# Kernel optimization log

Hardware: AMD Instinct MI355X
Metric: run time of the kernel (lower is better)

The kernel has to match this reference:

```python
import jax, jax.numpy as jnp
import numpy as np


def segsum(x):
    # x: (..., T). Returns (..., T, T) with out[l, s] = sum_{i=s+1..l} x[i] for s <= l, -inf above diagonal.
    T = x.shape[-1]
    cs = jnp.cumsum(x, axis=-1)
    diff = cs[..., :, None] - cs[..., None, :]
    mask = jnp.tril(jnp.ones((T, T), dtype=bool))
    return jnp.where(mask, diff, -jnp.inf)


def ssd_forward(X, A, B, C, block_len):
    # X: (b, s, h, p); A: (b, s, h); B, C: (b, s, h, n)
    b, s, h, p = X.shape
    n = B.shape[-1]
    nc = s // block_len  # number of chunks
    Xb = X.reshape(b, nc, block_len, h, p)
    Bb = B.reshape(b, nc, block_len, h, n)
    Cb = C.reshape(b, nc, block_len, h, n)
    Ab = A.reshape(b, nc, block_len, h).transpose(0, 3, 1, 2)  # (b, h, c, l)

    A_cumsum = jnp.cumsum(Ab, axis=-1)  # (b, h, c, l)

    # 1. Intra-chunk (diagonal block) outputs
    L = jnp.exp(segsum(Ab))  # (b, h, c, l, s)
    Y_diag = jnp.einsum('bclhn,bcshn,bhcls,bcshp->bclhp', Cb, Bb, L, Xb)

    # 2. Per-chunk final states
    decay_states = jnp.exp(A_cumsum[..., -1:] - A_cumsum)  # (b, h, c, l)
    states = jnp.einsum('bclhn,bhcl,bclhp->bchpn', Bb, decay_states, Xb)

    # 3. Inter-chunk scan (initial state = 0)
    init = jnp.zeros_like(states[:, :1])
    states_cat = jnp.concatenate([init, states], axis=1)  # (b, c+1, h, p, n)
    A_last = A_cumsum[..., -1]  # (b, h, c)
    A_padded = jnp.pad(A_last, ((0, 0), (0, 0), (1, 0)))  # (b, h, c+1)
    decay_chunk = jnp.exp(segsum(A_padded))  # (b, h, c+1, c+1)
    new_states = jnp.einsum('bhzc,bchpn->bzhpn', decay_chunk, states_cat)
    states_in = new_states[:, :-1]  # state entering each chunk, (b, c, h, p, n)

    # 4. Off-diagonal (inter-chunk) contribution to outputs
    state_decay_out = jnp.exp(A_cumsum)  # (b, h, c, l)
    Y_off = jnp.einsum('bclhn,bchpn,bhcl->bclhp', Cb, states_in, state_decay_out)

    return (Y_diag + Y_off).reshape(b, s, h, p)


def setup_inputs() -> dict:
    key = jax.random.key(0)
    k1, k2, k3, k4 = jax.random.split(key, 4)
    b, s, h, p, n = 16, 1024, 32, 64, 128
    X = jax.random.normal(k1, (b, s, h, p), dtype=jnp.float32)
    A = -jax.random.uniform(k2, (b, s, h), dtype=jnp.float32)  # negative decay (discretized dt*A)
    B = jax.random.normal(k3, (b, s, h, n), dtype=jnp.float32)
    C = jax.random.normal(k4, (b, s, h, n), dtype=jnp.float32)
    return {'X': X, 'A': A, 'B': B, 'C': C, 'block_len': 64}


def reference(X, A, B, C, block_len):
    return ssd_forward(X, A, B, C, block_len)
```

## Files before the change

### kernel.cpp

```cpp
#include <hip/hip_runtime.h>

typedef __attribute__((ext_vector_type(8))) __bf16 bf16x8;
typedef __attribute__((ext_vector_type(4))) __bf16 bf16x4;
typedef __attribute__((ext_vector_type(4))) float f32x4;

#define SEQ 1024
#define NH 32
#define PD 64
#define ND 128
#define CLEN 64
#define NCHUNK 16

#define CS_LD 136
#define BT_LD 72
#define XT_LD 72
#define SS_LD 72
#define SR_LD 136

__device__ __forceinline__ int swz(int r) { return ((r >> 2) & 7) << 3; }

__device__ __forceinline__ void barrier_lds() {
    asm volatile("s_waitcnt lgkmcnt(0)" ::: "memory");
    __builtin_amdgcn_s_barrier();
    asm volatile("" ::: "memory");
}

__global__ __launch_bounds__(512, 2)
void ssd_fused(const float* __restrict__ Xg, const float* __restrict__ Ag,
               const float* __restrict__ Bg, const float* __restrict__ Cg,
               float* __restrict__ Yg)
{
    __shared__ __align__(16) float cumA[64];
    __shared__ __align__(16) float eA[64];
    __shared__ __align__(16) float dxA[64];
    __shared__ __align__(16) float scal[4];
    __shared__ __align__(16) __bf16 Cs[64 * CS_LD];
    __shared__ __align__(16) __bf16 BsT[128 * BT_LD];
    __shared__ __align__(16) __bf16 XsT[64 * XT_LD];
    __shared__ __align__(16) __bf16 Ss[64 * SS_LD];
    __shared__ __align__(16) __bf16 SrB[64 * SR_LD];

    const int tid  = threadIdx.x;
    const int w    = tid >> 6;
    const int lane = tid & 63;
    const int q    = lane >> 4;
    const int ln   = lane & 15;
    const int m4   = w & 3;
    const int h2   = w >> 2;

    const int bh = blockIdx.x;
    const int b  = bh >> 5;
    const int h  = bh & 31;

    const float* Xb = Xg + (size_t)b * SEQ * NH * PD + (size_t)h * PD;
    const float* Ab = Ag + (size_t)b * SEQ * NH + h;
    const float* Bb = Bg + (size_t)b * SEQ * NH * ND + (size_t)h * ND;
    const float* Cb = Cg + (size_t)b * SEQ * NH * ND + (size_t)h * ND;
    float*       Yb = Yg + (size_t)b * SEQ * NH * PD + (size_t)h * PD;

    {
        unsigned int* p0 = (unsigned int*)SrB;
        for (int i = tid; i < 64 * SR_LD / 2; i += 512) p0[i] = 0u;
    }
    f32x4 srun[4];
    #pragma unroll
    for (int t = 0; t < 4; ++t) srun[t] = (f32x4){0.f, 0.f, 0.f, 0.f};
    __syncthreads();

    f32x4 creg[4], breg[4], xreg[2];
    float areg = 0.f;
    #define LOAD_CHUNK(S0) do {                                                   \
        _Pragma("unroll")                                                         \
        for (int i = 0; i < 4; ++i) {                                             \
            int v   = tid + 512 * i;                                              \
            int row = v >> 5;                                                     \
            int c4  = (v & 31) << 2;                                              \
            creg[i] = *(const f32x4*)(Cb + (size_t)((S0) + row) * (NH * ND) + c4);\
            breg[i] = *(const f32x4*)(Bb + (size_t)((S0) + row) * (NH * ND) + c4);\
        }                                                                         \
        _Pragma("unroll")                                                         \
        for (int i = 0; i < 2; ++i) {                                             \
            int v   = tid + 512 * i;                                              \
            int row = v >> 4;                                                     \
            int c4  = (v & 15) << 2;                                              \
            xreg[i] = *(const f32x4*)(Xb + (size_t)((S0) + row) * (NH * PD) + c4);\
        }                                                                         \
        if (w == 0) areg = Ab[(size_t)((S0) + lane) * NH];                        \
    } while (0)

    LOAD_CHUNK(0);

    for (int c = 0; c < NCHUNK; ++c) {
        const int s0 = c * CLEN;

        #pragma unroll
        for (int i = 0; i < 4; ++i) {
            int v   = tid + 512 * i;
            int row = v >> 5;
            int c4  = (v & 31) << 2;
            bf16x4 cv;
            cv[0] = (__bf16)creg[i][0]; cv[1] = (__bf16)creg[i][1];
            cv[2] = (__bf16)creg[i][2]; cv[3] = (__bf16)creg[i][3];
            *(bf16x4*)&Cs[row * CS_LD + c4] = cv;
            #pragma unroll
            for (int j = 0; j < 4; ++j) {
                int n = c4 + j;
                BsT[n * BT_LD + (row ^ swz(n))] = (__bf16)breg[i][j];
            }
        }
        #pragma unroll
        for (int i = 0; i < 2; ++i) {
            int v   = tid + 512 * i;
            int row = v >> 4;
            int c4  = (v & 15) << 2;
            #pragma unroll
            for (int j = 0; j < 4; ++j) {
                int p = c4 + j;
                XsT[p * XT_LD + (row ^ swz(p))] = (__bf16)xreg[i][j];
            }
        }

        if (w == 0) {
            float v = areg;
            #pragma unroll
            for (int off = 1; off < 64; off <<= 1) {
                float u = __shfl_up(v, off, 64);
                if (lane >= off) v += u;
            }
            float alast = __shfl(v, 63, 64);
            cumA[lane] = v;
            eA[lane]   = __expf(v);
            dxA[lane]  = __expf(alast - v);
            if (lane == 0) scal[0] = __expf(alast);
        }

        if (c + 1 < NCHUNK) LOAD_CHUNK((c + 1) * CLEN);

        barrier_lds();

        {
            const int arow = 16 * m4 + ln;
            f32x4 ca = *(const f32x4*)&cumA[16 * m4 + 4 * q];
            #pragma unroll
            for (int t = 0; t < 2; ++t) {
                const int sn   = 2 * h2 + t;
                const int scol = 16 * sn + ln;
                if (sn <= m4) {
                    f32x4 acc = (f32x4){0.f, 0.f, 0.f, 0.f};
                    #pragma unroll
                    for (int kt = 0; kt < 4; ++kt) {
                        bf16x8 af = *(const bf16x8*)&Cs[arow * CS_LD + kt * 32 + q * 8];
                        bf16x8 bq;
                        #pragma unroll
                        for (int j = 0; j < 8; ++j) {
                            int n = kt * 32 + q * 8 + j;
                            bq[j] = BsT[n * BT_LD + (scol ^ swz(n))];
                        }
                        acc = __builtin_amdgcn_mfma_f32_16x16x32_bf16(af, bq, acc, 0, 0, 0);
                    }
                    float csc = cumA[scol];
                    #pragma unroll
                    for (int r = 0; r < 4; ++r) {
                        int lrow  = 16 * m4 + 4 * q + r;
                        float val = (lrow >= scol) ? acc[r] * __expf(ca[r] - csc) : 0.f;
                        Ss[lrow * SS_LD + scol] = (__bf16)val;
                    }
                } else {
                    #pragma unroll
                    for (int r = 0; r < 4; ++r)
                        Ss[(16 * m4 + 4 * q + r) * SS_LD + scol] = (__bf16)0.f;
                }
            }
        }

        barrier_lds();

        f32x4 yacc[2], yoff[2];
        yacc[0] = (f32x4){0.f, 0.f, 0.f, 0.f};
        yacc[1] = (f32x4){0.f, 0.f, 0.f, 0.f};
        yoff[0] = (f32x4){0.f, 0.f, 0.f, 0.f};
        yoff[1] = (f32x4){0.f, 0.f, 0.f, 0.f};
        {
            const int arow = 16 * m4 + ln;
            for (int kt = 0; kt <= (m4 >> 1); ++kt) {
                bf16x8 af = *(const bf16x8*)&Ss[arow * SS_LD + kt * 32 + q * 8];
                #pragma unroll
                for (int t = 0; t < 2; ++t) {
                    int prow = 16 * (2 * h2 + t) + ln;
                    bf16x8 bq = *(const bf16x8*)&XsT[prow * XT_LD + ((kt * 32 + q * 8) ^ swz(prow))];
                    yacc[t] = __builtin_amdgcn_mfma_f32_16x16x32_bf16(af, bq, yacc[t], 0, 0, 0);
                }
            }
            #pragma unroll
            for (int kt = 0; kt < 4; ++kt) {
                bf16x8 craw = *(const bf16x8*)&Cs[arow * CS_LD + kt * 32 + q * 8];
                #pragma unroll
                for (int t = 0; t < 2; ++t) {
                    int pt = 2 * h2 + t;
                    bf16x8 bq = *(const bf16x8*)&SrB[(16 * pt + ln) * SR_LD + kt * 32 + q * 8];
                    yoff[t] = __builtin_amdgcn_mfma_f32_16x16x32_bf16(craw, bq, yoff[t], 0, 0, 0);
                }
            }
            f32x4 ev = *(const f32x4*)&eA[16 * m4 + 4 * q];
            #pragma unroll
            for (int t = 0; t < 2; ++t)
                #pragma unroll
                for (int r = 0; r < 4; ++r)
                    yacc[t][r] += ev[r] * yoff[t][r];
        }

        f32x4 sacc[4];
        #pragma unroll
        for (int t = 0; t < 4; ++t) sacc[t] = (f32x4){0.f, 0.f, 0.f, 0.f};
        {
            const int prow = 16 * m4 + ln;
            #pragma unroll
            for (int kt = 0; kt < 2; ++kt) {
                bf16x8 xv = *(const bf16x8*)&XsT[prow * XT_LD + ((kt * 32 + q * 8) ^ swz(prow))];
                f32x4 d0 = *(const f32x4*)&dxA[kt * 32 + q * 8];
                f32x4 d1 = *(const f32x4*)&dxA[kt * 32 + q * 8 + 4];
                bf16x8 af;
                #pragma unroll
                for (int j = 0; j < 4; ++j) {
                    af[j]     = (__bf16)((float)xv[j] * d0[j]);
                    af[4 + j] = (__bf16)((float)xv[4 + j] * d1[j]);
                }
                #pragma unroll
                for (int t = 0; t < 4; ++t) {
                    int nrow = 16 * (4 * h2 + t) + ln;
                    bf16x8 bq = *(const bf16x8*)&BsT[nrow * BT_LD + ((kt * 32 + q * 8) ^ swz(nrow))];
                    sacc[t] = __builtin_amdgcn_mfma_f32_16x16x32_bf16(af, bq, sacc[t], 0, 0, 0);
                }
            }
        }

        barrier_lds();

        {
            float elast = scal[0];
            #pragma unroll
            for (int t = 0; t < 4; ++t) {
                int ncol = 16 * (4 * h2 + t) + ln;
                #pragma unroll
                for (int r = 0; r < 4; ++r) {
                    float s = elast * srun[t][r] + sacc[t][r];
                    srun[t][r] = s;
                    SrB[(16 * m4 + 4 * q + r) * SR_LD + ncol] = (__bf16)s;
                }
            }
            #pragma unroll
            for (int t = 0; t < 2; ++t) {
                int pcol = 16 * (2 * h2 + t) + ln;
                #pragma unroll
                for (int r = 0; r < 4; ++r) {
                    int lrow = 16 * m4 + 4 * q + r;
                    Yb[(size_t)(s0 + lrow) * (NH * PD) + pcol] = yacc[t][r];
                }
            }
        }

        barrier_lds();
    }
    #undef LOAD_CHUNK
}

extern "C" void kernel_launch(void* const* d_in, const int* in_sizes, int n_in,
                              void* d_out, int out_size, void* d_ws, size_t ws_size,
                              hipStream_t stream) {
    const float* X = (const float*)d_in[0];
    const float* A = (const float*)d_in[1];
    const float* B = (const float*)d_in[2];
    const float* C = (const float*)d_in[3];
    float* Y = (float*)d_out;
    dim3 grid(512, 1, 1), block(512, 1, 1);
    hipLaunchKernelGGL(ssd_fused, grid, block, 0, stream, X, A, B, C, Y);
}
```

Baseline: 644.0 us.

## Load C fragments directly to registers and restructure chunk pipeline stages

C is no longer staged through shared memory; each lane loads its MFMA A-fragment rows of C straight from global memory into registers and converts them to bf16 there. B is now stored in both row-major and transposed shared layouts, so the C·Bᵀ product uses vector LDS reads instead of eight scalar gathers. The loop is reordered so that staging and the cumsum scan for the next chunk happen at the end of the current iteration, and the C prefetch is issued later, which moves one barrier. The occupancy hint in launch bounds rises from 2 to 4, which caps registers per thread more tightly and risks spills.

```diff
diff --git a/kernel.cpp b/kernel.cpp
--- a/kernel.cpp
+++ b/kernel.cpp
@@ -11,7 +11,7 @@
 #define CLEN 64
 #define NCHUNK 16
 
-#define CS_LD 136
+#define BS_LD 136
 #define BT_LD 72
 #define XT_LD 72
 #define SS_LD 72
@@ -25,7 +25,7 @@
     asm volatile("" ::: "memory");
 }
 
-__global__ __launch_bounds__(512, 2)
+__global__ __launch_bounds__(512, 4)
 void ssd_fused(const float* __restrict__ Xg, const float* __restrict__ Ag,
                const float* __restrict__ Bg, const float* __restrict__ Cg,
                float* __restrict__ Yg)
@@ -34,10 +34,10 @@
     __shared__ __align__(16) float eA[64];
     __shared__ __align__(16) float dxA[64];
     __shared__ __align__(16) float scal[4];
-    __shared__ __align__(16) __bf16 Cs[64 * CS_LD];
+    __shared__ __align__(16) __bf16 Bs [64 * BS_LD];
     __shared__ __align__(16) __bf16 BsT[128 * BT_LD];
     __shared__ __align__(16) __bf16 XsT[64 * XT_LD];
-    __shared__ __align__(16) __bf16 Ss[64 * SS_LD];
+    __shared__ __align__(16) __bf16 Ss [64 * SS_LD];
     __shared__ __align__(16) __bf16 SrB[64 * SR_LD];
 
     const int tid  = threadIdx.x;
@@ -58,6 +58,8 @@
     const float* Cb = Cg + (size_t)b * SEQ * NH * ND + (size_t)h * ND;
     float*       Yb = Yg + (size_t)b * SEQ * NH * PD + (size_t)h * PD;
 
+    const int arow = 16 * m4 + ln;
+
     {
         unsigned int* p0 = (unsigned int*)SrB;
         for (int i = tid; i < 64 * SR_LD / 2; i += 512) p0[i] = 0u;
@@ -65,17 +67,18 @@
     f32x4 srun[4];
     #pragma unroll
     for (int t = 0; t < 4; ++t) srun[t] = (f32x4){0.f, 0.f, 0.f, 0.f};
-    __syncthreads();
-
-    f32x4 creg[4], breg[4], xreg[2];
+
+    f32x4 breg[4], xreg[2];
     float areg = 0.f;
-    #define LOAD_CHUNK(S0) do {                                                   \
+    f32x4 cf32[8];
+    bf16x8 cfrag[4];
+
+    #define LOADBX(S0) do {                                                       \
         _Pragma("unroll")                                                         \
         for (int i = 0; i < 4; ++i) {                                             \
             int v   = tid + 512 * i;                                              \
             int row = v >> 5;                                                     \
             int c4  = (v & 31) << 2;                                              \
-            creg[i] = *(const f32x4*)(Cb + (size_t)((S0) + row) * (NH * ND) + c4);\
             breg[i] = *(const f32x4*)(Bb + (size_t)((S0) + row) * (NH * ND) + c4);\
         }                                                                         \
         _Pragma("unroll")                                                         \
@@ -88,59 +91,88 @@
         if (w == 0) areg = Ab[(size_t)((S0) + lane) * NH];                        \
     } while (0)
 
-    LOAD_CHUNK(0);
+    #define LOADC(S0) do {                                                        \
+        _Pragma("unroll")                                                         \
+        for (int kt = 0; kt < 4; ++kt) {                                          \
+            const float* p = Cb + (size_t)((S0) + arow) * (NH * ND) + kt * 32 + q * 8; \
+            cf32[2 * kt]     = *(const f32x4*)(p);                                \
+            cf32[2 * kt + 1] = *(const f32x4*)(p + 4);                            \
+        }                                                                         \
+    } while (0)
+
+    #define STAGE() do {                                                          \
+        _Pragma("unroll")                                                         \
+        for (int i = 0; i < 4; ++i) {                                             \
+            int v   = tid + 512 * i;                                              \
+            int row = v >> 5;                                                     \
+            int c4  = (v & 31) << 2;                                              \
+            bf16x4 bv;                                                            \
+            bv[0] = (__bf16)breg[i][0]; bv[1] = (__bf16)breg[i][1];               \
+            bv[2] = (__bf16)breg[i][2]; bv[3] = (__bf16)breg[i][3];               \
+            *(bf16x4*)&Bs[row * BS_LD + c4] = bv;                                 \
+            _Pragma("unroll")                                                     \
+            for (int j = 0; j < 4; ++j) {                                         \
+                int n = c4 + j;                                                   \
+                BsT[n * BT_LD + (row ^ swz(n))] = bv[j];                          \
+            }                                                                     \
+        }                                                                         \
+        _Pragma("unroll")                                                         \
+        for (int i = 0; i < 2; ++i) {                                             \
+            int v   = tid + 512 * i;                                              \
+            int row = v >> 4;                                                     \
+            int c4  = (v & 15) << 2;                                              \
+            _Pragma("unroll")                                                     \
+            for (int j = 0; j < 4; ++j) {                                         \
+                int p = c4 + j;                                                   \
+                XsT[p * XT_LD + (row ^ swz(p))] = (__bf16)xreg[i][j];             \
+            }                                                                     \
+        }                                                                         \
+    } while (0)
+
+    #define SCAN() do {                                                           \
+        if (w == 0) {                                                             \
+            float v = areg;                                                       \
+            _Pragma("unroll")                                                     \
+            for (int off = 1; off < 64; off <<= 1) {                              \
+                float u = __shfl_up(v, off, 64);                                  \
+                if (lane >= off) v += u;                                          \
+            }                                                                     \
+            float alast = __shfl(v, 63, 64);                                      \
+            cumA[lane] = v;                                                       \
+            eA[lane]   = __expf(v);                          \
+            dxA[lane]  = __expf(alast - v);                   \
+            if (lane == 0) scal[0] = __expf(alast);                               \
+        }                                                                         \
+    } while (0)
+
+    LOADBX(0);
+    LOADC(0);
+    STAGE();
+    SCAN();
 
     for (int c = 0; c < NCHUNK; ++c) {
         const int s0 = c * CLEN;
 
+        barrier_lds();
+
+        const float elast = scal[0];
+        const f32x4 ev = *(const f32x4*)&eA[16 * m4 + 4 * q];
+        const f32x4 ca = *(const f32x4*)&cumA[16 * m4 + 4 * q];
+
+        if (c + 1 < NCHUNK) LOADBX((c + 1) * CLEN);
+
         #pragma unroll
-        for (int i = 0; i < 4; ++i) {
-            int v   = tid + 512 * i;
-            int row = v >> 5;
-            int c4  = (v & 31) << 2;
-            bf16x4 cv;
-            cv[0] = (__bf16)creg[i][0]; cv[1] = (__bf16)creg[i][1];
-            cv[2] = (__bf16)creg[i][2]; cv[3] = (__bf16)creg[i][3];
-            *(bf16x4*)&Cs[row * CS_LD + c4] = cv;
+        for (int kt = 0; kt < 4; ++kt) {
+            bf16x8 f;
             #pragma unroll
             for (int j = 0; j < 4; ++j) {
-                int n = c4 + j;
-                BsT[n * BT_LD + (row ^ swz(n))] = (__bf16)breg[i][j];
-            }
-        }
-        #pragma unroll
-        for (int i = 0; i < 2; ++i) {
-            int v   = tid + 512 * i;
-            int row = v >> 4;
-            int c4  = (v & 15) << 2;
-            #pragma unroll
-            for (int j = 0; j < 4; ++j) {
-                int p = c4 + j;
-                XsT[p * XT_LD + (row ^ swz(p))] = (__bf16)xreg[i][j];
-            }
-        }
-
-        if (w == 0) {
-            float v = areg;
-            #pragma unroll
-            for (int off = 1; off < 64; off <<= 1) {
-                float u = __shfl_up(v, off, 64);
-                if (lane >= off) v += u;
-            }
-            float alast = __shfl(v, 63, 64);
-            cumA[lane] = v;
-            eA[lane]   = __expf(v);
-            dxA[lane]  = __expf(alast - v);
-            if (lane == 0) scal[0] = __expf(alast);
-        }
-
-        if (c + 1 < NCHUNK) LOAD_CHUNK((c + 1) * CLEN);
-
-        barrier_lds();
+                f[j]     = (__bf16)cf32[2 * kt][j];
+                f[4 + j] = (__bf16)cf32[2 * kt + 1][j];
+            }
+            cfrag[kt] = f;
+        }
 
         {
-            const int arow = 16 * m4 + ln;
-            f32x4 ca = *(const f32x4*)&cumA[16 * m4 + 4 * q];
             #pragma unroll
             for (int t = 0; t < 2; ++t) {
                 const int sn   = 2 * h2 + t;
@@ -149,14 +181,8 @@
                     f32x4 acc = (f32x4){0.f, 0.f, 0.f, 0.f};
                     #pragma unroll
                     for (int kt = 0; kt < 4; ++kt) {
-                        bf16x8 af = *(const bf16x8*)&Cs[arow * CS_LD + kt * 32 + q * 8];
-                        bf16x8 bq;
-                        #pragma unroll
-                        for (int j = 0; j < 8; ++j) {
-                            int n = kt * 32 + q * 8 + j;
-                            bq[j] = BsT[n * BT_LD + (scol ^ swz(n))];
-                        }
-                        acc = __builtin_amdgcn_mfma_f32_16x16x32_bf16(af, bq, acc, 0, 0, 0);
+                        bf16x8 bq = *(const bf16x8*)&Bs[scol * BS_LD + kt * 32 + q * 8];
+                        acc = __builtin_amdgcn_mfma_f32_16x16x32_bf16(cfrag[kt], bq, acc, 0, 0, 0);
                     }
                     float csc = cumA[scol];
                     #pragma unroll
@@ -173,47 +199,24 @@
             }
         }
 
-        barrier_lds();
-
-        f32x4 yacc[2], yoff[2];
-        yacc[0] = (f32x4){0.f, 0.f, 0.f, 0.f};
-        yacc[1] = (f32x4){0.f, 0.f, 0.f, 0.f};
+        f32x4 yoff[2];
         yoff[0] = (f32x4){0.f, 0.f, 0.f, 0.f};
         yoff[1] = (f32x4){0.f, 0.f, 0.f, 0.f};
-        {
-            const int arow = 16 * m4 + ln;
-            for (int kt = 0; kt <= (m4 >> 1); ++kt) {
-                bf16x8 af = *(const bf16x8*)&Ss[arow * SS_LD + kt * 32 + q * 8];
-                #pragma unroll
-                for (int t = 0; t < 2; ++t) {
-                    int prow = 16 * (2 * h2 + t) + ln;
-                    bf16x8 bq = *(const bf16x8*)&XsT[prow * XT_LD + ((kt * 32 + q * 8) ^ swz(prow))];
-                    yacc[t] = __builtin_amdgcn_mfma_f32_16x16x32_bf16(af, bq, yacc[t], 0, 0, 0);
-                }
-            }
-            #pragma unroll
-            for (int kt = 0; kt < 4; ++kt) {
-                bf16x8 craw = *(const bf16x8*)&Cs[arow * CS_LD + kt * 32 + q * 8];
-                #pragma unroll
-                for (int t = 0; t < 2; ++t) {
-                    int pt = 2 * h2 + t;
-                    bf16x8 bq = *(const bf16x8*)&SrB[(16 * pt + ln) * SR_LD + kt * 32 + q * 8];
-                    yoff[t] = __builtin_amdgcn_mfma_f32_16x16x32_bf16(craw, bq, yoff[t], 0, 0, 0);
-                }
-            }
-            f32x4 ev = *(const f32x4*)&eA[16 * m4 + 4 * q];
-            #pragma unroll
-            for (int t = 0; t < 2; ++t)
-                #pragma unroll
-                for (int r = 0; r < 4; ++r)
-                    yacc[t][r] += ev[r] * yoff[t][r];
+        #pragma unroll
+        for (int kt = 0; kt < 4; ++kt) {
+            #pragma unroll
+            for (int t = 0; t < 2; ++t) {
+                int pt = 2 * h2 + t;
+                bf16x8 bq = *(const bf16x8*)&SrB[(16 * pt + ln) * SR_LD + kt * 32 + q * 8];
+                yoff[t] = __builtin_amdgcn_mfma_f32_16x16x32_bf16(cfrag[kt], bq, yoff[t], 0, 0, 0);
+            }
         }
 
         f32x4 sacc[4];
         #pragma unroll
         for (int t = 0; t < 4; ++t) sacc[t] = (f32x4){0.f, 0.f, 0.f, 0.f};
         {
-            const int prow = 16 * m4 + ln;
+            const int prow = arow;
             #pragma unroll
             for (int kt = 0; kt < 2; ++kt) {
                 bf16x8 xv = *(const bf16x8*)&XsT[prow * XT_LD + ((kt * 32 + q * 8) ^ swz(prow))];
@@ -236,8 +239,31 @@
 
         barrier_lds();
 
+        if (c + 1 < NCHUNK) LOADC((c + 1) * CLEN);
+
+        f32x4 yacc[2];
+        yacc[0] = (f32x4){0.f, 0.f, 0.f, 0.f};
+        yacc[1] = (f32x4){0.f, 0.f, 0.f, 0.f};
         {
-            float elast = scal[0];
+            for (int kt = 0; kt <= (m4 >> 1); ++kt) {
+                bf16x8 af = *(const bf16x8*)&Ss[arow * SS_LD + kt * 32 + q * 8];
+                #pragma unroll
+                for (int t = 0; t < 2; ++t) {
+                    int prow = 16 * (2 * h2 + t) + ln;
+                    bf16x8 bq = *(const bf16x8*)&XsT[prow * XT_LD + ((kt * 32 + q * 8) ^ swz(prow))];
+                    yacc[t] = __builtin_amdgcn_mfma_f32_16x16x32_bf16(af, bq, yacc[t], 0, 0, 0);
+                }
+            }
+            #pragma unroll
+            for (int t = 0; t < 2; ++t)
+                #pragma unroll
+                for (int r = 0; r < 4; ++r)
+                    yacc[t][r] += ev[r] * yoff[t][r];
+        }
+
+        barrier_lds();
+
+        {
             #pragma unroll
             for (int t = 0; t < 4; ++t) {
                 int ncol = 16 * (4 * h2 + t) + ln;
@@ -259,9 +285,15 @@
             }
         }
 
-        barrier_lds();
+        if (c + 1 < NCHUNK) {
+            STAGE();
+            SCAN();
+        }
     }
-    #undef LOAD_CHUNK
+    #undef LOADBX
+    #undef LOADC
+    #undef STAGE
+    #undef SCAN
 }
 
 extern "C" void kernel_launch(void* const* d_in, const int* in_sizes, int n_in,
```

After: 802.4 us. 24.6% more time.
